# Optimization experiments

Measured on AMD Instinct MI355X. Metric: run time of the kernel, lower is better.

Reference implementation:

```python
import jax, jax.numpy as jnp
import numpy as np

H = 8        # num_heads
DK = 128     # head_k_dim
DV = 128     # head_v_dim
HID = 1024   # hidden_size
CHUNK = 64   # chunk size for chunked linear attention
EPS = 1e-5


def setup_inputs() -> dict:
    key = jax.random.key(0)
    ks = jax.random.split(key, 16)
    s = 0.02
    inp = {
        "hidden_states": jax.random.normal(ks[0], (2, 8192, HID), dtype=jnp.float32),
        "Wq": jax.random.normal(ks[1], (HID, HID), dtype=jnp.float32) * s,
        "Wk": jax.random.normal(ks[2], (HID, HID), dtype=jnp.float32) * s,
        "Wv": jax.random.normal(ks[3], (HID, HID), dtype=jnp.float32) * s,
        "fmq_w1": jax.random.normal(ks[4], (DK, DK), dtype=jnp.float32) * s,
        "fmq_b1": jnp.zeros((DK,), dtype=jnp.float32),
        "fmq_w2": jax.random.normal(ks[5], (DK, DK), dtype=jnp.float32) * s,
        "fmq_b2": jnp.zeros((DK,), dtype=jnp.float32),
        "fmk_w1": jax.random.normal(ks[6], (DK, DK), dtype=jnp.float32) * s,
        "fmk_b1": jnp.zeros((DK,), dtype=jnp.float32),
        "fmk_w2": jax.random.normal(ks[7], (DK, DK), dtype=jnp.float32) * s,
        "fmk_b2": jnp.zeros((DK,), dtype=jnp.float32),
        "rms_w": jnp.ones((DV,), dtype=jnp.float32),
        "Wo": jax.random.normal(ks[8], (HID, HID), dtype=jnp.float32) * s,
    }
    return inp


def reference(hidden_states, Wq, Wk, Wv, fmq_w1, fmq_b1, fmq_w2, fmq_b2,
              fmk_w1, fmk_b1, fmk_w2, fmk_b2, rms_w, Wo):
    B, T, _ = hidden_states.shape
    scale = DK ** -0.5

    # projections (torch Linear: x @ W.T), split heads -> [B,T,H,D]
    q = (hidden_states @ Wq.T).reshape(B, T, H, DK)
    k = (hidden_states @ Wk.T).reshape(B, T, H, DK)
    v = (hidden_states @ Wv.T).reshape(B, T, H, DV)

    # Hadamard feature maps: l1(x) * l2(x)
    q = (q @ fmq_w1.T + fmq_b1) * (q @ fmq_w2.T + fmq_b2)
    k = (k @ fmk_w1.T + fmk_b1) * (k @ fmk_w2.T + fmk_b2)

    q = q * scale

    # chunked causal linear attention: o_t = q_t @ sum_{s<=t} k_s v_s^T
    N = T // CHUNK
    qc = q.reshape(B, N, CHUNK, H, DK)
    kc = k.reshape(B, N, CHUNK, H, DK)
    vc = v.reshape(B, N, CHUNK, H, DV)

    # per-chunk KV outer-product sums, exclusive prefix over chunks
    kv = jnp.einsum('bnchk,bnchv->bnhkv', kc, vc)
    S = jnp.cumsum(kv, axis=1) - kv  # state entering each chunk

    o_inter = jnp.einsum('bnchk,bnhkv->bnchv', qc, S)

    # intra-chunk causal part
    A = jnp.einsum('bnihk,bnjhk->bnhij', qc, kc)
    causal = jnp.tril(jnp.ones((CHUNK, CHUNK), dtype=bool))
    A = jnp.where(causal, A, 0.0)
    o_intra = jnp.einsum('bnhij,bnjhv->bnihv', A, vc)

    o = (o_inter + o_intra).reshape(B, T, H, DV)

    # RMSNorm over head_v_dim with affine weight
    o = o * jax.lax.rsqrt(jnp.mean(o * o, axis=-1, keepdims=True) + EPS) * rms_w

    o = o.reshape(B, T, H * DV) @ Wo.T
    return o
```

## Files before the change

kernel.cpp:

```cpp
#include <hip/hip_runtime.h>


typedef __bf16 bf16x8 __attribute__((ext_vector_type(8)));
typedef float  f32x4  __attribute__((ext_vector_type(4)));

__device__ __forceinline__ float bf2f(unsigned short u) {
  union { unsigned int i; float f; } v; v.i = ((unsigned int)u) << 16; return v.f;
}
__device__ __forceinline__ unsigned short f2bf(float f) {
  union { float f; unsigned int i; } v; v.f = f;
  return (unsigned short)((v.i + 0x8000u) >> 16);
}
__device__ __forceinline__ unsigned int pk2(float a, float b) {
  union { float f; unsigned int i; } x, y; x.f = a; y.f = b;
  return ((x.i + 0x8000u) >> 16) | ((y.i + 0x8000u) & 0xFFFF0000u);
}
__device__ __forceinline__ f32x4 mfma16(bf16x8 a, bf16x8 b, f32x4 c) {
  return __builtin_amdgcn_mfma_f32_16x16x32_bf16(a, b, c, 0, 0, 0);
}
__device__ __forceinline__ void gl_lds16(const unsigned short* g, unsigned short* l) {
  __builtin_amdgcn_global_load_lds((const __attribute__((address_space(1))) void*)g,
                                   (__attribute__((address_space(3))) void*)l, 16, 0, 0);
}

__global__ void __launch_bounds__(256)
cvt_all(const float* __restrict__ X,
        const float* __restrict__ W0, const float* __restrict__ W1,
        const float* __restrict__ W2, const float* __restrict__ W3,
        const float* __restrict__ F0, const float* __restrict__ F1,
        const float* __restrict__ F2, const float* __restrict__ F3,
        unsigned short* __restrict__ Xd,
        unsigned short* __restrict__ W0d, unsigned short* __restrict__ W1d,
        unsigned short* __restrict__ W2d, unsigned short* __restrict__ W3d,
        unsigned short* __restrict__ F0d, unsigned short* __restrict__ F1d,
        unsigned short* __restrict__ F2d, unsigned short* __restrict__ F3d) {
  const int i = blockIdx.x * 256 + threadIdx.x;
  const float* s; unsigned short* d; int off;
  if (i < 4194304) { s = X; d = Xd; off = i; }
  else {
    int i2 = i - 4194304;
    if (i2 < 1048576) {
      const int w = i2 >> 18; off = i2 & 262143;
      s = (w == 0) ? W0 : (w == 1) ? W1 : (w == 2) ? W2 : W3;
      d = (w == 0) ? W0d : (w == 1) ? W1d : (w == 2) ? W2d : W3d;
    } else {
      int i3 = i2 - 1048576;
      if (i3 >= 16384) return;
      const int w = i3 >> 12; off = i3 & 4095;
      s = (w == 0) ? F0 : (w == 1) ? F1 : (w == 2) ? F2 : F3;
      d = (w == 0) ? F0d : (w == 1) ? F1d : (w == 2) ? F2d : F3d;
    }
  }
  const float4 f = ((const float4*)s)[off];
  uint2 o; o.x = pk2(f.x, f.y); o.y = pk2(f.z, f.w);
  ((uint2*)d)[off] = o;
}

__device__ __forceinline__ int stage_goff(int s) {
  const int j = s >> 3, c = (s & 7) ^ (j & 7);
  return (2 * j + (c >> 2)) * 1024 + (c & 3) * 8;
}

__device__ __forceinline__ void gemm256_loop(const unsigned short* __restrict__ gA,
                                             const unsigned short* __restrict__ gB,
                                             unsigned short* __restrict__ ldsA,
                                             unsigned short* __restrict__ ldsB,
                                             int tid, f32x4 (&acc)[8][4]) {
  const int lane = tid & 63, wid = tid >> 6;
  const int lq = lane & 15, quad = lane >> 4;
  const int wm = (wid >> 2) * 128, wn = (wid & 3) * 64;

  const unsigned short* gA0 = gA + stage_goff(tid);
  const unsigned short* gA1 = gA + stage_goff(512 + tid);
  const unsigned short* gB0 = gB + stage_goff(tid);
  const unsigned short* gB1 = gB + stage_goff(512 + tid);
  const int l0 = wid * 512;
  const int l1 = 4096 + wid * 512;
  const int soff = (lq >> 1) * 64 + (((((lq & 1) << 2) + quad) ^ ((lq >> 1) & 7))) * 8;

#pragma unroll
  for (int h = 0; h < 3; ++h) {
    gl_lds16(gA0 + h * 32, ldsA + h * 8192 + l0);
    gl_lds16(gA1 + h * 32, ldsA + h * 8192 + l1);
    gl_lds16(gB0 + h * 32, ldsB + h * 8192 + l0);
    gl_lds16(gB1 + h * 32, ldsB + h * 8192 + l1);
  }
  asm volatile("s_waitcnt vmcnt(4)" ::: "memory");
  __builtin_amdgcn_s_barrier();
  __builtin_amdgcn_sched_barrier(0);

  bf16x8 pa[2][8], pb[2][4];
#pragma unroll
  for (int f = 0; f < 8; ++f)
    pa[0][f] = *(const bf16x8*)(ldsA + (wm + f * 16) * 32 + soff);
#pragma unroll
  for (int g = 0; g < 4; ++g)
    pb[0][g] = *(const bf16x8*)(ldsB + (wn + g * 16) * 32 + soff);

#pragma unroll
  for (int u = 0; u < 32; ++u) {
    const int cur = u & 1, nxt = cur ^ 1;
    if (u > 0) {
      if (u < 30) asm volatile("s_waitcnt vmcnt(4)" ::: "memory");
      else        asm volatile("s_waitcnt vmcnt(0)" ::: "memory");
      __builtin_amdgcn_s_barrier();
      __builtin_amdgcn_sched_barrier(0);
    }
    if (u < 29) {
      unsigned short* sa = ldsA + ((u + 3) & 3) * 8192;
      unsigned short* sb = ldsB + ((u + 3) & 3) * 8192;
      gl_lds16(gA0 + (u + 3) * 32, sa + l0);
      gl_lds16(gA1 + (u + 3) * 32, sa + l1);
      gl_lds16(gB0 + (u + 3) * 32, sb + l0);
      gl_lds16(gB1 + (u + 3) * 32, sb + l1);
    }
    if (u < 31) {
      const unsigned short* An = ldsA + ((u + 1) & 3) * 8192;
      const unsigned short* Bn = ldsB + ((u + 1) & 3) * 8192;
#pragma unroll
      for (int f = 0; f < 8; ++f)
        pa[nxt][f] = *(const bf16x8*)(An + (wm + f * 16) * 32 + soff);
#pragma unroll
      for (int g = 0; g < 4; ++g)
        pb[nxt][g] = *(const bf16x8*)(Bn + (wn + g * 16) * 32 + soff);
    }
    __builtin_amdgcn_s_setprio(1);
#pragma unroll
    for (int f = 0; f < 8; ++f)
#pragma unroll
      for (int g = 0; g < 4; ++g)
        acc[f][g] = mfma16(pa[cur][f], pb[cur][g], acc[f][g]);
    __builtin_amdgcn_s_setprio(0);
  }
}

__global__ void __launch_bounds__(512, 2)
qkv_gemm256(const unsigned short* __restrict__ Xb, const unsigned short* __restrict__ Bw,
            unsigned short* __restrict__ Cq, unsigned short* __restrict__ VT, int sel) {
  extern __shared__ unsigned short lds[];
  const int tid = threadIdx.x;
  const int bx = blockIdx.x;
  const int tm = (bx & 7) * 8 + ((bx >> 3) & 7);
  const int ct = bx >> 6;
  const int rowBase = tm * 256, colBase = ct * 256;

  f32x4 acc[8][4] = {};
  gemm256_loop(Xb + (size_t)rowBase * 1024, Bw + (size_t)colBase * 1024,
               lds, lds + 32768, tid, acc);

  const int lane = tid & 63, wid = tid >> 6;
  const int lq = lane & 15, quad = lane >> 4;
  const int wm = (wid >> 2) * 128, wn = (wid & 3) * 64;
  if (sel < 2) {
#pragma unroll
    for (int f = 0; f < 8; ++f)
#pragma unroll
      for (int g = 0; g < 4; ++g) {
        const int col = colBase + wn + g * 16 + lq;
#pragma unroll
        for (int r = 0; r < 4; ++r) {
          const int row = rowBase + wm + f * 16 + quad * 4 + r;
          Cq[(size_t)row * 1024 + col] = f2bf(acc[f][g][r]);
        }
      }
  } else {
#pragma unroll
    for (int f = 0; f < 8; ++f)
#pragma unroll
      for (int g = 0; g < 4; ++g) {
        const int col = colBase + wn + g * 16 + lq;
        const int h = col >> 7, dv = col & 127;
        const int row0 = rowBase + wm + f * 16 + quad * 4;
        const int b = row0 >> 13, tl = row0 & 8191;
        ushort4 t4;
        t4.x = f2bf(acc[f][g][0]); t4.y = f2bf(acc[f][g][1]);
        t4.z = f2bf(acc[f][g][2]); t4.w = f2bf(acc[f][g][3]);
        *(ushort4*)(VT + (((size_t)(b * 8 + h) * 128 + dv) << 13) + tl) = t4;
      }
  }
}

__global__ void __launch_bounds__(512, 2)
out_gemm256(const unsigned short* __restrict__ A, const unsigned short* __restrict__ Bw,
            float* __restrict__ C) {
  extern __shared__ unsigned short lds[];
  const int tid = threadIdx.x;
  const int bx = blockIdx.x;
  const int tm = (bx & 7) * 8 + ((bx >> 3) & 7);
  const int tn = bx >> 6;
  const int rowBase = tm * 256, colBase = tn * 256;

  f32x4 acc[8][4] = {};
  gemm256_loop(A + (size_t)rowBase * 1024, Bw + (size_t)colBase * 1024,
               lds, lds + 32768, tid, acc);

  const int lane = tid & 63, wid = tid >> 6;
  const int lq = lane & 15, quad = lane >> 4;
  const int wm = (wid >> 2) * 128, wn = (wid & 3) * 64;
#pragma unroll
  for (int f = 0; f < 8; ++f)
#pragma unroll
    for (int g = 0; g < 4; ++g) {
      const int col = colBase + wn + g * 16 + lq;
#pragma unroll
      for (int r = 0; r < 4; ++r) {
        const int row = rowBase + wm + f * 16 + quad * 4 + r;
        C[(size_t)row * 1024 + col] = acc[f][g][r];
      }
    }
}

__global__ void __launch_bounds__(256)
fm_kernel(unsigned short* __restrict__ Qb, unsigned short* __restrict__ Kb,
          const unsigned short* __restrict__ fq1b, const unsigned short* __restrict__ fq2b,
          const unsigned short* __restrict__ fk1b, const unsigned short* __restrict__ fk2b,
          const float* __restrict__ fqb1, const float* __restrict__ fqb2,
          const float* __restrict__ fkb1, const float* __restrict__ fkb2) {
  __shared__ unsigned short Aq[64 * 136];
  const int z = blockIdx.z;
  unsigned short* buf = z ? Kb : Qb;
  const unsigned short* w1b = z ? fk1b : fq1b;
  const unsigned short* w2b = z ? fk2b : fq2b;
  const float* b1 = z ? fkb1 : fqb1;
  const float* b2 = z ? fkb2 : fqb2;
  const float scale = z ? 1.0f : 0.08838834764831843f;

  const int tid = threadIdx.x;
  const int t0 = blockIdx.x * 256;
  const int h = blockIdx.y, hc = h * 128;
  const int lane = tid & 63, wid = tid >> 6, lq = lane & 15, quad = lane >> 4;
  const int wn = wid * 32;

  bf16x8 w1f[4][2], w2f[4][2];
#pragma unroll
  for (int ks = 0; ks < 4; ++ks)
#pragma unroll
    for (int j = 0; j < 2; ++j) {
      const int nr = wn + j * 16 + lq;
      w1f[ks][j] = *(const bf16x8*)(w1b + nr * 128 + ks * 32 + quad * 8);
      w2f[ks][j] = *(const bf16x8*)(w2b + nr * 128 + ks * 32 + quad * 8);
    }

  const float bb1[2] = { b1[wn + lq], b1[wn + 16 + lq] };
  const float bb2[2] = { b2[wn + lq], b2[wn + 16 + lq] };

  for (int tt = 0; tt < 4; ++tt) {
    const int tb = t0 + tt * 64;
#pragma unroll
    for (int it = 0; it < 4; ++it) {
      const int p = tid + it * 256;
      const int row = p >> 4, c8 = (p & 15) * 8;
      *(uint4*)(Aq + row * 136 + c8) =
          *(const uint4*)(buf + (size_t)(tb + row) * 1024 + hc + c8);
    }
    __syncthreads();
    f32x4 a1[4][2] = {}, a2[4][2] = {};
#pragma unroll
    for (int ks = 0; ks < 4; ++ks) {
      bf16x8 af[4];
#pragma unroll
      for (int i = 0; i < 4; ++i)
        af[i] = *(const bf16x8*)(Aq + (i * 16 + lq) * 136 + ks * 32 + quad * 8);
#pragma unroll
      for (int j = 0; j < 2; ++j)
#pragma unroll
        for (int i = 0; i < 4; ++i) {
          a1[i][j] = mfma16(af[i], w1f[ks][j], a1[i][j]);
          a2[i][j] = mfma16(af[i], w2f[ks][j], a2[i][j]);
        }
    }
    __syncthreads();
#pragma unroll
    for (int j = 0; j < 2; ++j) {
      const int col = wn + j * 16 + lq;
#pragma unroll
      for (int i = 0; i < 4; ++i)
#pragma unroll
        for (int r = 0; r < 4; ++r) {
          const float v = (a1[i][j][r] + bb1[j]) * (a2[i][j][r] + bb2[j]) * scale;
          buf[(size_t)(tb + i * 16 + quad * 4 + r) * 1024 + hc + col] = f2bf(v);
        }
    }
  }
}

__global__ void __launch_bounds__(256)
kv_kernel(const unsigned short* __restrict__ Kf, const unsigned short* __restrict__ VT,
          unsigned short* __restrict__ KV) {
  __shared__ unsigned short Kt[128 * 72];
  __shared__ unsigned short Vt[128 * 72];
  const int tid = threadIdx.x;
  const int n = blockIdx.x, bh = blockIdx.y;
  const int b = bh >> 3, h = bh & 7;
  const int t0g = b * 8192 + n * 64;
  const int tl0 = n * 64;
#pragma unroll
  for (int it = 0; it < 4; ++it) {
    const int p = tid + it * 256;
    const int d = p >> 3, c8 = (p & 7) * 8;
    *(uint4*)(Vt + d * 72 + c8) =
        *(const uint4*)(VT + (((size_t)bh * 128 + d) << 13) + tl0 + c8);
    const int tok = p >> 4, c8k = (p & 15) * 8;
    const unsigned short* src = Kf + (size_t)(t0g + tok) * 1024 + h * 128 + c8k;
    ushort4 k0 = *(const ushort4*)(src);
    ushort4 k1 = *(const ushort4*)(src + 4);
    Kt[(c8k + 0) * 72 + tok] = k0.x; Kt[(c8k + 1) * 72 + tok] = k0.y;
    Kt[(c8k + 2) * 72 + tok] = k0.z; Kt[(c8k + 3) * 72 + tok] = k0.w;
    Kt[(c8k + 4) * 72 + tok] = k1.x; Kt[(c8k + 5) * 72 + tok] = k1.y;
    Kt[(c8k + 6) * 72 + tok] = k1.z; Kt[(c8k + 7) * 72 + tok] = k1.w;
  }
  __syncthreads();
  const int lane = tid & 63, wid = tid >> 6, lq = lane & 15, quad = lane >> 4;
  const int wm = (wid >> 1) * 64, wn = (wid & 1) * 64;
  f32x4 acc[4][4] = {};
#pragma unroll
  for (int ks = 0; ks < 2; ++ks) {
    bf16x8 af[4], bfr[4];
#pragma unroll
    for (int i = 0; i < 4; ++i)
      af[i] = *(const bf16x8*)(Vt + (wm + i * 16 + lq) * 72 + ks * 32 + quad * 8);
#pragma unroll
    for (int j = 0; j < 4; ++j)
      bfr[j] = *(const bf16x8*)(Kt + (wn + j * 16 + lq) * 72 + ks * 32 + quad * 8);
#pragma unroll
    for (int i = 0; i < 4; ++i)
#pragma unroll
      for (int j = 0; j < 4; ++j) acc[i][j] = mfma16(af[i], bfr[j], acc[i][j]);
  }
  const size_t base = ((size_t)bh * 128 + n) * 16384;
#pragma unroll
  for (int i = 0; i < 4; ++i)
#pragma unroll
    for (int j = 0; j < 4; ++j)
#pragma unroll
      for (int r = 0; r < 4; ++r)
        KV[base + (size_t)(wm + i * 16 + quad * 4 + r) * 128 + wn + j * 16 + lq] =
            f2bf(acc[i][j][r]);
}

__global__ void __launch_bounds__(256)
cumsum_kernel(unsigned short* __restrict__ KV) {
  const int idx = blockIdx.x * 256 + threadIdx.x;
  const int bh = idx >> 14, e = idx & 16383;
  unsigned short* p = KV + (size_t)bh * (128 * 16384) + e;
  float run = 0.f;
  for (int nb = 0; nb < 16; ++nb) {
    unsigned short x[8];
#pragma unroll
    for (int i = 0; i < 8; ++i) x[i] = p[(size_t)i * 16384];
#pragma unroll
    for (int i = 0; i < 8; ++i) {
      const float v = bf2f(x[i]);
      p[(size_t)i * 16384] = f2bf(run);
      run += v;
    }
    p += (size_t)8 * 16384;
  }
}

__global__ void __launch_bounds__(256)
attn_kernel(const unsigned short* __restrict__ Q, const unsigned short* __restrict__ Kf,
            const unsigned short* __restrict__ VT, const unsigned short* __restrict__ S,
            const float* __restrict__ rmsw, unsigned short* __restrict__ O) {
  __shared__ uint4 smem4[3968];
  unsigned short* sm = (unsigned short*)smem4;
  unsigned short* SQ = sm;
  unsigned short* KS = sm + 8704;
  unsigned short* VTl = sm + 17920;
  unsigned short* AL = sm + 27136;
  float* OL = (float*)sm;
  float* RED = (float*)AL;
  float* SCL = RED + 256;

  const int tid = threadIdx.x;
  const int n = blockIdx.x, bh = blockIdx.y;
  const int b = bh >> 3, h = bh & 7;
  const int t0g = b * 8192 + n * 64;
  const int tl0 = n * 64;
  const int lane = tid & 63, wid = tid >> 6, lq = lane & 15, quad = lane >> 4;

  const size_t sbase = ((size_t)bh * 128 + n) * 16384;
  bf16x8 sfr[2][2][2];
#pragma unroll
  for (int hh = 0; hh < 2; ++hh)
#pragma unroll
    for (int ks = 0; ks < 2; ++ks)
#pragma unroll
      for (int j = 0; j < 2; ++j)
        sfr[hh][ks][j] = *(const bf16x8*)(S + sbase +
            (size_t)(wid * 32 + j * 16 + lq) * 128 + hh * 64 + ks * 32 + quad * 8);

#pragma unroll
  for (int it = 0; it < 4; ++it) {
    const int p = tid + it * 256;
    const int row = p >> 4, c8 = (p & 15) * 8;
    *(uint4*)(SQ + row * 136 + c8) =
        *(const uint4*)(Q + (size_t)(t0g + row) * 1024 + h * 128 + c8);
    *(uint4*)(KS + row * 136 + c8) =
        *(const uint4*)(Kf + (size_t)(t0g + row) * 1024 + h * 128 + c8);
    const int d = p >> 3, c8b = (p & 7) * 8;
    *(uint4*)(VTl + d * 72 + c8b) =
        *(const uint4*)(VT + (((size_t)bh * 128 + d) << 13) + tl0 + c8b);
  }
  __syncthreads();

  {
    f32x4 aa[4] = {};
#pragma unroll
    for (int ks = 0; ks < 4; ++ks) {
      bf16x8 kf = *(const bf16x8*)(KS + (wid * 16 + lq) * 136 + ks * 32 + quad * 8);
#pragma unroll
      for (int i = 0; i < 4; ++i) {
        bf16x8 qf = *(const bf16x8*)(SQ + (i * 16 + lq) * 136 + ks * 32 + quad * 8);
        aa[i] = mfma16(qf, kf, aa[i]);
      }
    }
#pragma unroll
    for (int i = 0; i < 4; ++i)
#pragma unroll
      for (int r = 0; r < 4; ++r) {
        const int qp = i * 16 + quad * 4 + r, kp = wid * 16 + lq;
        AL[qp * 72 + kp] = f2bf(kp <= qp ? aa[i][r] : 0.f);
      }
  }
  __syncthreads();

  f32x4 oa[4][2] = {};
#pragma unroll
  for (int ks = 0; ks < 2; ++ks) {
    bf16x8 bv[2];
#pragma unroll
    for (int j = 0; j < 2; ++j)
      bv[j] = *(const bf16x8*)(VTl + (wid * 32 + j * 16 + lq) * 72 + ks * 32 + quad * 8);
#pragma unroll
    for (int i = 0; i < 4; ++i) {
      bf16x8 af  = *(const bf16x8*)(AL + (i * 16 + lq) * 72 + ks * 32 + quad * 8);
      bf16x8 qf0 = *(const bf16x8*)(SQ + (i * 16 + lq) * 136 + ks * 32 + quad * 8);
      bf16x8 qf1 = *(const bf16x8*)(SQ + (i * 16 + lq) * 136 + (ks + 2) * 32 + quad * 8);
#pragma unroll
      for (int j = 0; j < 2; ++j) {
        oa[i][j] = mfma16(af, bv[j], oa[i][j]);
        oa[i][j] = mfma16(qf0, sfr[0][ks][j], oa[i][j]);
        oa[i][j] = mfma16(qf1, sfr[1][ks][j], oa[i][j]);
      }
    }
  }
  __syncthreads();

#pragma unroll
  for (int i = 0; i < 4; ++i)
#pragma unroll
    for (int j = 0; j < 2; ++j)
#pragma unroll
      for (int r = 0; r < 4; ++r)
        OL[(i * 16 + quad * 4 + r) * 132 + wid * 32 + j * 16 + lq] = oa[i][j][r];
  __syncthreads();

  {
    const int r = tid >> 2, part = tid & 3;
    const float* pr = OL + r * 132 + part * 32;
    float s = 0.f;
#pragma unroll
    for (int c = 0; c < 32; ++c) { const float v = pr[c]; s += v * v; }
    RED[r * 4 + part] = s;
  }
  __syncthreads();
  if (tid < 64) {
    const float ms = (RED[tid * 4] + RED[tid * 4 + 1] + RED[tid * 4 + 2] + RED[tid * 4 + 3]) *
                     (1.f / 128.f);
    SCL[tid] = rsqrtf(ms + 1e-5f);
  }
  __syncthreads();

#pragma unroll
  for (int it = 0; it < 4; ++it) {
    const int r = (tid >> 4) + it * 16;
    const int c8 = (tid & 15) * 8;
    const float sc = SCL[r];
    unsigned short us[8];
#pragma unroll
    for (int e = 0; e < 8; ++e)
      us[e] = f2bf(OL[r * 132 + c8 + e] * sc * rmsw[c8 + e]);
    uint4 pk;
    pk.x = (unsigned int)us[0] | ((unsigned int)us[1] << 16);
    pk.y = (unsigned int)us[2] | ((unsigned int)us[3] << 16);
    pk.z = (unsigned int)us[4] | ((unsigned int)us[5] << 16);
    pk.w = (unsigned int)us[6] | ((unsigned int)us[7] << 16);
    *(uint4*)(O + (size_t)(t0g + r) * 1024 + h * 128 + c8) = pk;
  }
}

extern "C" void kernel_launch(void* const* d_in, const int* in_sizes, int n_in,
                              void* d_out, int out_size, void* d_ws, size_t ws_size,
                              hipStream_t stream) {
  const float* X    = (const float*)d_in[0];
  const float* Wq   = (const float*)d_in[1];
  const float* Wk   = (const float*)d_in[2];
  const float* Wv   = (const float*)d_in[3];
  const float* fq1  = (const float*)d_in[4];
  const float* fqb1 = (const float*)d_in[5];
  const float* fq2  = (const float*)d_in[6];
  const float* fqb2 = (const float*)d_in[7];
  const float* fk1  = (const float*)d_in[8];
  const float* fkb1 = (const float*)d_in[9];
  const float* fk2  = (const float*)d_in[10];
  const float* fkb2 = (const float*)d_in[11];
  const float* rmsw = (const float*)d_in[12];
  const float* Wo   = (const float*)d_in[13];

  static bool attr_done = false;
  if (!attr_done) {
    (void)hipFuncSetAttribute((const void*)qkv_gemm256,
                              hipFuncAttributeMaxDynamicSharedMemorySize, 131072);
    (void)hipFuncSetAttribute((const void*)out_gemm256,
                              hipFuncAttributeMaxDynamicSharedMemorySize, 131072);
    attr_done = true;
  }

  const size_t MB = 1u << 20;
  char* ws = (char*)d_ws;
  unsigned short* Q    = (unsigned short*)(ws);
  unsigned short* Kf   = (unsigned short*)(ws + 32 * MB);
  unsigned short* VT   = (unsigned short*)(ws + 64 * MB);
  unsigned short* KV   = (unsigned short*)(ws + 96 * MB);
  unsigned short* Xb   = KV;
  unsigned short* Wqb  = (unsigned short*)(ws + 160 * MB);
  unsigned short* Wkb  = (unsigned short*)(ws + 162 * MB);
  unsigned short* Wvb  = (unsigned short*)(ws + 164 * MB);
  unsigned short* Wob  = (unsigned short*)(ws + 166 * MB);
  unsigned short* fq1b = (unsigned short*)(ws + 168 * MB);
  unsigned short* fq2b = fq1b + 16384;
  unsigned short* fk1b = fq1b + 32768;
  unsigned short* fk2b = fq1b + 49152;
  unsigned short* O    = Q;

  cvt_all<<<20544, 256, 0, stream>>>(X, Wq, Wk, Wv, Wo, fq1, fq2, fk1, fk2,
                                     Xb, Wqb, Wkb, Wvb, Wob,
                                     fq1b, fq2b, fk1b, fk2b);

  qkv_gemm256<<<dim3(256), dim3(512), 131072, stream>>>(Xb, Wqb, Q, VT, 0);
  qkv_gemm256<<<dim3(256), dim3(512), 131072, stream>>>(Xb, Wkb, Kf, VT, 1);
  qkv_gemm256<<<dim3(256), dim3(512), 131072, stream>>>(Xb, Wvb, Q, VT, 2);
  fm_kernel<<<dim3(64, 8, 2), 256, 0, stream>>>(Q, Kf, fq1b, fq2b, fk1b, fk2b,
                                                fqb1, fqb2, fkb1, fkb2);
  kv_kernel<<<dim3(128, 16), 256, 0, stream>>>(Kf, VT, KV);
  cumsum_kernel<<<1024, 256, 0, stream>>>(KV);
  attn_kernel<<<dim3(128, 16), 256, 0, stream>>>(Q, Kf, VT, KV, rmsw, O);
  out_gemm256<<<dim3(256), dim3(512), 131072, stream>>>(O, Wob, (float*)d_out);
}
```

Baseline: 394.7 us.

## Merge Q/K/V GEMMs into one launch and retile output GEMM to 128x128

The three separate Q, K and V projection GEMM launches become a single 768-block launch that picks its weight matrix and output from the block index. This removes two launch boundaries and lets all three projections share the machine at once, cutting tail idle time. The output projection moves from 256x256 tiles with 512 threads (256 blocks) to a new 128x128-tile kernel with 256 threads and 1024 blocks. It has its own 4-stage global-to-LDS pipeline, aimed at better CU occupancy and load balance on a GEMM that only had 256 blocks. Smaller tiles mean less data reuse per block and more global traffic for the output GEMM.

New measurement: 416.0 us. +5.4%, slower.

```diff
diff --git a/kernel.cpp b/kernel.cpp
--- a/kernel.cpp
+++ b/kernel.cpp
@@ -135,14 +135,19 @@
 }
 
 __global__ void __launch_bounds__(512, 2)
-qkv_gemm256(const unsigned short* __restrict__ Xb, const unsigned short* __restrict__ Bw,
-            unsigned short* __restrict__ Cq, unsigned short* __restrict__ VT, int sel) {
+qkv_gemm256(const unsigned short* __restrict__ Xb,
+            const unsigned short* __restrict__ Wqb, const unsigned short* __restrict__ Wkb,
+            const unsigned short* __restrict__ Wvb,
+            unsigned short* __restrict__ Q, unsigned short* __restrict__ Kf,
+            unsigned short* __restrict__ VT) {
   extern __shared__ unsigned short lds[];
   const int tid = threadIdx.x;
   const int bx = blockIdx.x;
   const int tm = (bx & 7) * 8 + ((bx >> 3) & 7);
   const int ct = bx >> 6;
-  const int rowBase = tm * 256, colBase = ct * 256;
+  const int sel = ct >> 2;
+  const int rowBase = tm * 256, colBase = (ct & 3) * 256;
+  const unsigned short* Bw = (sel == 0) ? Wqb : ((sel == 1) ? Wkb : Wvb);
 
   f32x4 acc[8][4] = {};
   gemm256_loop(Xb + (size_t)rowBase * 1024, Bw + (size_t)colBase * 1024,
@@ -152,6 +157,7 @@
   const int lq = lane & 15, quad = lane >> 4;
   const int wm = (wid >> 2) * 128, wn = (wid & 3) * 64;
   if (sel < 2) {
+    unsigned short* C = (sel == 0) ? Q : Kf;
 #pragma unroll
     for (int f = 0; f < 8; ++f)
 #pragma unroll
@@ -160,7 +166,7 @@
 #pragma unroll
         for (int r = 0; r < 4; ++r) {
           const int row = rowBase + wm + f * 16 + quad * 4 + r;
-          Cq[(size_t)row * 1024 + col] = f2bf(acc[f][g][r]);
+          C[(size_t)row * 1024 + col] = f2bf(acc[f][g][r]);
         }
       }
   } else {
@@ -180,25 +186,88 @@
   }
 }
 
-__global__ void __launch_bounds__(512, 2)
-out_gemm256(const unsigned short* __restrict__ A, const unsigned short* __restrict__ Bw,
+__global__ void __launch_bounds__(256)
+out_gemm128(const unsigned short* __restrict__ A, const unsigned short* __restrict__ Bw,
             float* __restrict__ C) {
   extern __shared__ unsigned short lds[];
+  unsigned short* ldsA = lds;
+  unsigned short* ldsB = lds + 16384;
   const int tid = threadIdx.x;
   const int bx = blockIdx.x;
-  const int tm = (bx & 7) * 8 + ((bx >> 3) & 7);
-  const int tn = bx >> 6;
-  const int rowBase = tm * 256, colBase = tn * 256;
-
-  f32x4 acc[8][4] = {};
-  gemm256_loop(A + (size_t)rowBase * 1024, Bw + (size_t)colBase * 1024,
-               lds, lds + 32768, tid, acc);
+  const int l = (bx & 7) * 128 + (bx >> 3);
+  const int tm = l & 127, tn = l >> 7;
+  const int rowBase = tm * 128, colBase = tn * 128;
+  const unsigned short* gAt = A + (size_t)rowBase * 1024;
+  const unsigned short* gBt = Bw + (size_t)colBase * 1024;
 
   const int lane = tid & 63, wid = tid >> 6;
   const int lq = lane & 15, quad = lane >> 4;
-  const int wm = (wid >> 2) * 128, wn = (wid & 3) * 64;
-#pragma unroll
-  for (int f = 0; f < 8; ++f)
+  const int wm = (wid >> 1) * 64, wn = (wid & 1) * 64;
+
+  const unsigned short* gA0 = gAt + stage_goff(tid);
+  const unsigned short* gA1 = gAt + stage_goff(256 + tid);
+  const unsigned short* gB0 = gBt + stage_goff(tid);
+  const unsigned short* gB1 = gBt + stage_goff(256 + tid);
+  const int l0 = wid * 512;
+  const int l1 = 2048 + wid * 512;
+  const int soff = (lq >> 1) * 64 + (((((lq & 1) << 2) + quad) ^ ((lq >> 1) & 7))) * 8;
+
+  f32x4 acc[4][4] = {};
+#pragma unroll
+  for (int h = 0; h < 3; ++h) {
+    gl_lds16(gA0 + h * 32, ldsA + h * 4096 + l0);
+    gl_lds16(gA1 + h * 32, ldsA + h * 4096 + l1);
+    gl_lds16(gB0 + h * 32, ldsB + h * 4096 + l0);
+    gl_lds16(gB1 + h * 32, ldsB + h * 4096 + l1);
+  }
+  asm volatile("s_waitcnt vmcnt(4)" ::: "memory");
+  __builtin_amdgcn_s_barrier();
+  __builtin_amdgcn_sched_barrier(0);
+
+  bf16x8 pa[2][4], pb[2][4];
+#pragma unroll
+  for (int f = 0; f < 4; ++f) {
+    pa[0][f] = *(const bf16x8*)(ldsA + (wm + f * 16) * 32 + soff);
+    pb[0][f] = *(const bf16x8*)(ldsB + (wn + f * 16) * 32 + soff);
+  }
+
+#pragma unroll
+  for (int u = 0; u < 32; ++u) {
+    const int cur = u & 1, nxt = cur ^ 1;
+    if (u > 0) {
+      if (u < 30) asm volatile("s_waitcnt vmcnt(4)" ::: "memory");
+      else        asm volatile("s_waitcnt vmcnt(0)" ::: "memory");
+      __builtin_amdgcn_s_barrier();
+      __builtin_amdgcn_sched_barrier(0);
+    }
+    if (u < 29) {
+      unsigned short* sa = ldsA + ((u + 3) & 3) * 4096;
+      unsigned short* sb = ldsB + ((u + 3) & 3) * 4096;
+      gl_lds16(gA0 + (u + 3) * 32, sa + l0);
+      gl_lds16(gA1 + (u + 3) * 32, sa + l1);
+      gl_lds16(gB0 + (u + 3) * 32, sb + l0);
+      gl_lds16(gB1 + (u + 3) * 32, sb + l1);
+    }
+    if (u < 31) {
+      const unsigned short* An = ldsA + ((u + 1) & 3) * 4096;
+      const unsigned short* Bn = ldsB + ((u + 1) & 3) * 4096;
+#pragma unroll
+      for (int f = 0; f < 4; ++f) {
+        pa[nxt][f] = *(const bf16x8*)(An + (wm + f * 16) * 32 + soff);
+        pb[nxt][f] = *(const bf16x8*)(Bn + (wn + f * 16) * 32 + soff);
+      }
+    }
+    __builtin_amdgcn_s_setprio(1);
+#pragma unroll
+    for (int f = 0; f < 4; ++f)
+#pragma unroll
+      for (int g = 0; g < 4; ++g)
+        acc[f][g] = mfma16(pa[cur][f], pb[cur][g], acc[f][g]);
+    __builtin_amdgcn_s_setprio(0);
+  }
+
+#pragma unroll
+  for (int f = 0; f < 4; ++f)
 #pragma unroll
     for (int g = 0; g < 4; ++g) {
       const int col = colBase + wn + g * 16 + lq;
@@ -512,8 +581,8 @@
   if (!attr_done) {
     (void)hipFuncSetAttribute((const void*)qkv_gemm256,
                               hipFuncAttributeMaxDynamicSharedMemorySize, 131072);
-    (void)hipFuncSetAttribute((const void*)out_gemm256,
-                              hipFuncAttributeMaxDynamicSharedMemorySize, 131072);
+    (void)hipFuncSetAttribute((const void*)out_gemm128,
+                              hipFuncAttributeMaxDynamicSharedMemorySize, 65536);
     attr_done = true;
   }
 
@@ -538,13 +607,11 @@
                                      Xb, Wqb, Wkb, Wvb, Wob,
                                      fq1b, fq2b, fk1b, fk2b);
 
-  qkv_gemm256<<<dim3(256), dim3(512), 131072, stream>>>(Xb, Wqb, Q, VT, 0);
-  qkv_gemm256<<<dim3(256), dim3(512), 131072, stream>>>(Xb, Wkb, Kf, VT, 1);
-  qkv_gemm256<<<dim3(256), dim3(512), 131072, stream>>>(Xb, Wvb, Q, VT, 2);
+  qkv_gemm256<<<dim3(768), dim3(512), 131072, stream>>>(Xb, Wqb, Wkb, Wvb, Q, Kf, VT);
   fm_kernel<<<dim3(64, 8, 2), 256, 0, stream>>>(Q, Kf, fq1b, fq2b, fk1b, fk2b,
                                                 fqb1, fqb2, fkb1, fkb2);
   kv_kernel<<<dim3(128, 16), 256, 0, stream>>>(Kf, VT, KV);
   cumsum_kernel<<<1024, 256, 0, stream>>>(KV);
   attn_kernel<<<dim3(128, 16), 256, 0, stream>>>(Q, Kf, VT, KV, rmsw, O);
-  out_gemm256<<<dim3(256), dim3(512), 131072, stream>>>(O, Wob, (float*)d_out);
-}
+  out_gemm128<<<dim3(1024), dim3(256), 65536, stream>>>(O, Wob, (float*)d_out);
+}
```
